# Optimization experiments

Hardware: AMD Instinct MI355X
Metric: run time of the kernel (lower is better)

Reference implementation:

```python
import jax, jax.numpy as jnp
import numpy as np

# DeltaNet single-token decode step. Hard-coded dims from the torch source:
# hidden H=2048 (chosen), qk=2048 (16h x 128 -> repeat to 32h), v=4096 (32h x 128),
# conv channels 8192, kernel 4, state [1,32,128,128].
H = 2048
EPS = 1e-6

def _l2norm(x):
    return x * jax.lax.rsqrt(jnp.sum(x * x, axis=-1, keepdims=True) + EPS)

def setup_inputs() -> dict:
    key = jax.random.key(0)
    ks = jax.random.split(key, 12)
    w = lambda k, s, sc=0.02: jax.random.normal(k, s, dtype=jnp.float32) * sc
    return {
        "x": jax.random.normal(ks[0], (1, 1, H), dtype=jnp.float32),
        "state": jax.random.normal(ks[1], (1, 32, 128, 128), dtype=jnp.float32) * 0.02,
        "conv_state": jax.random.normal(ks[2], (1, 8192, 3), dtype=jnp.float32) * 0.1,
        "W_qkv": w(ks[3], (8192, H)),
        "W_z": w(ks[4], (4096, H)),
        "W_b": w(ks[5], (32, H)),
        "W_a": w(ks[6], (32, H)),
        "conv_w": w(ks[7], (8192, 1, 4), 0.3),
        "A_log": jax.random.uniform(ks[8], (32,), minval=-2.0, maxval=0.0, dtype=jnp.float32),
        "dt_bias": w(ks[9], (32,), 0.5),
        "norm_w": jnp.ones((128,), jnp.float32),
        "W_out": w(ks[10], (H, 4096)),
    }

def reference(x, state, conv_state, W_qkv, W_z, W_b, W_a, conv_w, A_log, dt_bias, norm_w, W_out):
    # projections (bias-free Linear, torch convention y = x @ W.T)
    mixed = jnp.einsum('blh,ch->blc', x, W_qkv)           # [1,1,8192]
    z = jnp.einsum('blh,ch->blc', x, W_z).reshape(1, 1, 32, 128)
    beta = jax.nn.sigmoid(jnp.einsum('blh,ch->blc', x, W_b))  # [1,1,32]
    a = jnp.einsum('blh,ch->blc', x, W_a)                 # [1,1,32]

    # depthwise causal conv (groups=8192, kernel 4, output length 1)
    combined = jnp.concatenate([conv_state, mixed.transpose(0, 2, 1)], axis=-1)  # [1,8192,4]
    new_conv = combined[:, :, -3:]
    conv_out = jnp.sum(combined * conv_w[None, :, 0, :], axis=-1)  # [1,8192]
    mixed = jax.nn.silu(conv_out)[:, None, :]             # [1,1,8192]

    q, k, v = mixed[..., :2048], mixed[..., 2048:4096], mixed[..., 4096:]
    q = jnp.repeat(q.reshape(1, 1, 16, 128), 2, axis=2)   # [1,1,32,128]
    k = jnp.repeat(k.reshape(1, 1, 16, 128), 2, axis=2)
    v = v.reshape(1, 1, 32, 128)

    g = -jnp.exp(A_log) * jax.nn.softplus(a + dt_bias)    # [1,1,32]

    q = _l2norm(q)[:, 0] / jnp.sqrt(jnp.float32(128.0))   # [1,32,128]
    k = _l2norm(k)[:, 0]
    v = v[:, 0]
    g_t = jnp.exp(g[:, 0])[..., None, None]               # [1,32,1,1]
    beta_t = beta[:, 0][..., None]                        # [1,32,1]

    # gated delta-rule state update
    s = state * g_t                                       # [1,32,128,128]
    kv_mem = jnp.einsum('bhkv,bhk->bhv', s, k)            # [1,32,128]
    delta = (v - kv_mem) * beta_t
    new_state = s + k[..., None] * delta[..., None, :]    # [1,32,128,128]
    out = jnp.einsum('bhkv,bhk->bhv', new_state, q)       # [1,32,128]

    # gated RMSNorm (Mamba2-style: rmsnorm(x * silu(z)) * w)
    out_flat = out.reshape(-1, 128)
    z_flat = z.reshape(-1, 128)
    gated = out_flat * jax.nn.silu(z_flat)
    out_flat = gated * jax.lax.rsqrt(jnp.mean(gated * gated, axis=-1, keepdims=True) + EPS) * norm_w

    out = jnp.einsum('blc,hc->blh', out_flat.reshape(1, 1, 4096), W_out)  # [1,1,H]
    return (out, new_state, new_conv)
```

## Files before the change

kernel.cpp:

```cpp
#include <hip/hip_runtime.h>
#include <math.h>

__global__ __launch_bounds__(256) void k_gemv_in(
    const float* __restrict__ x,
    const float* __restrict__ Wqkv,
    const float* __restrict__ Wz,
    const float* __restrict__ Wb,
    const float* __restrict__ Wa,
    float* __restrict__ mixed, float* __restrict__ zb,
    float* __restrict__ b_raw, float* __restrict__ a_raw)
{
  const int tid  = threadIdx.x;
  const int lane = tid & 63;
  const int wave = tid >> 6;

  float4 xr[8];
  #pragma unroll
  for (int j = 0; j < 8; j++)
    xr[j] = *(const float4*)(x + j*256 + lane*4);

  const int row0 = blockIdx.x * 16 + wave * 4;
  for (int rr = 0; rr < 4; rr++){
    const int row = row0 + rr;
    const float* W; float* dst;
    if (row < 8192)       { W = Wqkv + (size_t)row * 2048;          dst = mixed + row; }
    else if (row < 12288) { W = Wz   + (size_t)(row-8192) * 2048;   dst = zb + (row-8192); }
    else if (row < 12320) { W = Wb   + (size_t)(row-12288) * 2048;  dst = b_raw + (row-12288); }
    else                  { W = Wa   + (size_t)(row-12320) * 2048;  dst = a_raw + (row-12320); }
    float acc = 0.f;
    #pragma unroll
    for (int j = 0; j < 8; j++){
      float4 w = *(const float4*)(W + j*256 + lane*4);
      acc += w.x*xr[j].x + w.y*xr[j].y + w.z*xr[j].z + w.w*xr[j].w;
    }
    #pragma unroll
    for (int off = 32; off >= 1; off >>= 1) acc += __shfl_xor(acc, off, 64);
    if (lane == 0) *dst = acc;
  }
}

__global__ __launch_bounds__(256) void k_conv(
    const float* __restrict__ conv_state,
    const float* __restrict__ conv_w,
    const float* __restrict__ mixed,
    float* __restrict__ act,
    float* __restrict__ new_conv)
{
  const int c = blockIdx.x * 256 + threadIdx.x;
  const float cs0 = conv_state[c*3+0];
  const float cs1 = conv_state[c*3+1];
  const float cs2 = conv_state[c*3+2];
  const float m   = mixed[c];
  const float w0 = conv_w[c*4+0];
  const float w1 = conv_w[c*4+1];
  const float w2 = conv_w[c*4+2];
  const float w3 = conv_w[c*4+3];
  const float co = cs0*w0 + cs1*w1 + cs2*w2 + m*w3;
  act[c] = co / (1.f + expf(-co));
  new_conv[c*3+0] = cs1;
  new_conv[c*3+1] = cs2;
  new_conv[c*3+2] = m;
}

__global__ __launch_bounds__(128) void k_head(
    const float* __restrict__ act,
    const float* __restrict__ zbuf,
    const float* __restrict__ b_raw,
    const float* __restrict__ a_raw,
    const float* __restrict__ A_log,
    const float* __restrict__ dt_bias,
    const float* __restrict__ norm_w,
    const float* __restrict__ state,
    float* __restrict__ new_state,
    float* __restrict__ out_flat)
{
  const int h = blockIdx.x;
  const int t = threadIdx.x;
  const int hb = h >> 1;
  const int lane = t & 63, wid = t >> 6;

  __shared__ float qn[128], kn[128];
  __shared__ float red[4];

  const float qv = act[hb*128 + t];
  const float kv = act[2048 + hb*128 + t];
  const float vv = act[4096 + h*128 + t];

  float sq = qv*qv, sk = kv*kv;
  #pragma unroll
  for (int off = 32; off >= 1; off >>= 1){
    sq += __shfl_xor(sq, off, 64);
    sk += __shfl_xor(sk, off, 64);
  }
  if (lane == 0){ red[wid] = sq; red[2+wid] = sk; }
  __syncthreads();
  const float qscale = rsqrtf(red[0]+red[1] + 1e-6f) * 0.088388347648318440550f;
  const float kscale = rsqrtf(red[2]+red[3] + 1e-6f);
  qn[t] = qv * qscale;
  kn[t] = kv * kscale;
  __syncthreads();

  float g_t, beta;
  {
    const float av = a_raw[h] + dt_bias[h];
    const float sp = (av > 20.f) ? av : log1pf(expf(av));
    g_t  = expf(-expf(A_log[h]) * sp);
    beta = 1.f / (1.f + expf(-b_raw[h]));
  }

  const float* st  = state     + (size_t)h * 16384;
  float*       nst = new_state + (size_t)h * 16384;

  float s[128];
  float kvm = 0.f;
  #pragma unroll
  for (int k = 0; k < 128; k++){
    s[k] = st[k*128 + t] * g_t;
    kvm += s[k] * kn[k];
  }
  const float delta = (vv - kvm) * beta;
  float oacc = 0.f;
  #pragma unroll
  for (int k = 0; k < 128; k++){
    const float ns = s[k] + kn[k] * delta;
    nst[k*128 + t] = ns;
    oacc += ns * qn[k];
  }

  const float zz = zbuf[h*128 + t];
  const float gated = oacc * (zz / (1.f + expf(-zz)));
  float s2 = gated * gated;
  #pragma unroll
  for (int off = 32; off >= 1; off >>= 1) s2 += __shfl_xor(s2, off, 64);
  if (lane == 0) red[wid] = s2;
  __syncthreads();
  const float mean = (red[0] + red[1]) * (1.f/128.f);
  out_flat[h*128 + t] = gated * rsqrtf(mean + 1e-6f) * norm_w[t];
}

__global__ __launch_bounds__(256) void k_gemv_out(
    const float* __restrict__ out_flat,
    const float* __restrict__ Wout,
    float* __restrict__ out)
{
  __shared__ float xs[4096];
  const int tid = threadIdx.x;
  #pragma unroll
  for (int i = 0; i < 16; i++) xs[tid + i*256] = out_flat[tid + i*256];
  __syncthreads();

  const int lane = tid & 63, wave = tid >> 6;
  const int row0 = blockIdx.x * 16 + wave * 4;
  for (int rr = 0; rr < 4; rr++){
    const int row = row0 + rr;
    const float* W = Wout + (size_t)row * 4096;
    float acc = 0.f;
    #pragma unroll
    for (int j = 0; j < 16; j++){
      float4 w = *(const float4*)(W + j*256 + lane*4);
      acc += w.x*xs[j*256+lane*4+0] + w.y*xs[j*256+lane*4+1]
           + w.z*xs[j*256+lane*4+2] + w.w*xs[j*256+lane*4+3];
    }
    #pragma unroll
    for (int off = 32; off >= 1; off >>= 1) acc += __shfl_xor(acc, off, 64);
    if (lane == 0) out[row] = acc;
  }
}

extern "C" void kernel_launch(void* const* d_in, const int* in_sizes, int n_in,
                              void* d_out, int out_size, void* d_ws, size_t ws_size,
                              hipStream_t stream) {
  const float* x          = (const float*)d_in[0];
  const float* state      = (const float*)d_in[1];
  const float* conv_state = (const float*)d_in[2];
  const float* W_qkv      = (const float*)d_in[3];
  const float* W_z        = (const float*)d_in[4];
  const float* W_b        = (const float*)d_in[5];
  const float* W_a        = (const float*)d_in[6];
  const float* conv_w     = (const float*)d_in[7];
  const float* A_log      = (const float*)d_in[8];
  const float* dt_bias    = (const float*)d_in[9];
  const float* norm_w     = (const float*)d_in[10];
  const float* W_out      = (const float*)d_in[11];

  float* out       = (float*)d_out;
  float* new_state = (float*)d_out + 2048;
  float* new_conv  = (float*)d_out + 2048 + 524288;

  float* ws     = (float*)d_ws;
  float* mixed  = ws;
  float* zb     = ws + 8192;
  float* b_raw  = ws + 12288;
  float* a_raw  = ws + 12320;
  float* act    = ws + 12352;
  float* oflat  = ws + 20544;

  hipLaunchKernelGGL(k_gemv_in, dim3(772), dim3(256), 0, stream,
                     x, W_qkv, W_z, W_b, W_a, mixed, zb, b_raw, a_raw);
  hipLaunchKernelGGL(k_conv, dim3(32), dim3(256), 0, stream,
                     conv_state, conv_w, mixed, act, new_conv);
  hipLaunchKernelGGL(k_head, dim3(32), dim3(128), 0, stream,
                     act, zb, b_raw, a_raw, A_log, dt_bias, norm_w,
                     state, new_state, oflat);
  hipLaunchKernelGGL(k_gemv_out, dim3(128), dim3(256), 0, stream,
                     oflat, W_out, out);
}
```

Baseline: 193.3 us.

## Fuse depthwise conv into head kernel and widen GEMV grids with two rows per wave

The separate conv kernel is removed. Each head block now computes the conv and SiLU for its own q, k and v channels and writes new_conv itself, which saves one launch and the round trip through the act buffer. Both GEMV kernels now have each wave handle two rows at once with both weight loads in flight, and the grids are doubled so more waves stream the weight matrices. The cost is that q/k conv channels are computed twice, once by each head that shares them, and the head kernel, which still runs only 32 blocks, gets more serial work.

```diff
diff --git a/kernel.cpp b/kernel.cpp
--- a/kernel.cpp
+++ b/kernel.cpp
@@ -19,51 +19,33 @@
   for (int j = 0; j < 8; j++)
     xr[j] = *(const float4*)(x + j*256 + lane*4);
 
-  const int row0 = blockIdx.x * 16 + wave * 4;
-  for (int rr = 0; rr < 4; rr++){
-    const int row = row0 + rr;
-    const float* W; float* dst;
-    if (row < 8192)       { W = Wqkv + (size_t)row * 2048;          dst = mixed + row; }
-    else if (row < 12288) { W = Wz   + (size_t)(row-8192) * 2048;   dst = zb + (row-8192); }
-    else if (row < 12320) { W = Wb   + (size_t)(row-12288) * 2048;  dst = b_raw + (row-12288); }
-    else                  { W = Wa   + (size_t)(row-12320) * 2048;  dst = a_raw + (row-12320); }
-    float acc = 0.f;
-    #pragma unroll
-    for (int j = 0; j < 8; j++){
-      float4 w = *(const float4*)(W + j*256 + lane*4);
-      acc += w.x*xr[j].x + w.y*xr[j].y + w.z*xr[j].z + w.w*xr[j].w;
-    }
-    #pragma unroll
-    for (int off = 32; off >= 1; off >>= 1) acc += __shfl_xor(acc, off, 64);
-    if (lane == 0) *dst = acc;
-  }
-}
-
-__global__ __launch_bounds__(256) void k_conv(
+  const int row0 = blockIdx.x * 8 + wave * 2;
+  const float* W; float* dst;
+  if (row0 < 8192)       { W = Wqkv + (size_t)row0 * 2048;          dst = mixed + row0; }
+  else if (row0 < 12288) { W = Wz   + (size_t)(row0-8192) * 2048;   dst = zb + (row0-8192); }
+  else if (row0 < 12320) { W = Wb   + (size_t)(row0-12288) * 2048;  dst = b_raw + (row0-12288); }
+  else                   { W = Wa   + (size_t)(row0-12320) * 2048;  dst = a_raw + (row0-12320); }
+
+  float acc0 = 0.f, acc1 = 0.f;
+  #pragma unroll
+  for (int j = 0; j < 8; j++){
+    float4 w0 = *(const float4*)(W + j*256 + lane*4);
+    float4 w1 = *(const float4*)(W + 2048 + j*256 + lane*4);
+    acc0 += w0.x*xr[j].x + w0.y*xr[j].y + w0.z*xr[j].z + w0.w*xr[j].w;
+    acc1 += w1.x*xr[j].x + w1.y*xr[j].y + w1.z*xr[j].z + w1.w*xr[j].w;
+  }
+  #pragma unroll
+  for (int off = 32; off >= 1; off >>= 1){
+    acc0 += __shfl_xor(acc0, off, 64);
+    acc1 += __shfl_xor(acc1, off, 64);
+  }
+  if (lane == 0){ dst[0] = acc0; dst[1] = acc1; }
+}
+
+__global__ __launch_bounds__(128) void k_head(
+    const float* __restrict__ mixed,
     const float* __restrict__ conv_state,
     const float* __restrict__ conv_w,
-    const float* __restrict__ mixed,
-    float* __restrict__ act,
-    float* __restrict__ new_conv)
-{
-  const int c = blockIdx.x * 256 + threadIdx.x;
-  const float cs0 = conv_state[c*3+0];
-  const float cs1 = conv_state[c*3+1];
-  const float cs2 = conv_state[c*3+2];
-  const float m   = mixed[c];
-  const float w0 = conv_w[c*4+0];
-  const float w1 = conv_w[c*4+1];
-  const float w2 = conv_w[c*4+2];
-  const float w3 = conv_w[c*4+3];
-  const float co = cs0*w0 + cs1*w1 + cs2*w2 + m*w3;
-  act[c] = co / (1.f + expf(-co));
-  new_conv[c*3+0] = cs1;
-  new_conv[c*3+1] = cs2;
-  new_conv[c*3+2] = m;
-}
-
-__global__ __launch_bounds__(128) void k_head(
-    const float* __restrict__ act,
     const float* __restrict__ zbuf,
     const float* __restrict__ b_raw,
     const float* __restrict__ a_raw,
@@ -72,6 +54,7 @@
     const float* __restrict__ norm_w,
     const float* __restrict__ state,
     float* __restrict__ new_state,
+    float* __restrict__ new_conv,
     float* __restrict__ out_flat)
 {
   const int h = blockIdx.x;
@@ -82,9 +65,31 @@
   __shared__ float qn[128], kn[128];
   __shared__ float red[4];
 
-  const float qv = act[hb*128 + t];
-  const float kv = act[2048 + hb*128 + t];
-  const float vv = act[4096 + h*128 + t];
+  const int cq = hb*128 + t;
+  const int ck = 2048 + hb*128 + t;
+  const int cv = 4096 + h*128 + t;
+  float qv, kv, vv;
+  {
+    float c0, c1, c2, m, w0, w1, w2, w3, co;
+    c0 = conv_state[cq*3+0]; c1 = conv_state[cq*3+1]; c2 = conv_state[cq*3+2];
+    m  = mixed[cq];
+    w0 = conv_w[cq*4+0]; w1 = conv_w[cq*4+1]; w2 = conv_w[cq*4+2]; w3 = conv_w[cq*4+3];
+    co = c0*w0 + c1*w1 + c2*w2 + m*w3;
+    qv = co / (1.f + expf(-co));
+    new_conv[cq*3+0] = c1; new_conv[cq*3+1] = c2; new_conv[cq*3+2] = m;
+    c0 = conv_state[ck*3+0]; c1 = conv_state[ck*3+1]; c2 = conv_state[ck*3+2];
+    m  = mixed[ck];
+    w0 = conv_w[ck*4+0]; w1 = conv_w[ck*4+1]; w2 = conv_w[ck*4+2]; w3 = conv_w[ck*4+3];
+    co = c0*w0 + c1*w1 + c2*w2 + m*w3;
+    kv = co / (1.f + expf(-co));
+    new_conv[ck*3+0] = c1; new_conv[ck*3+1] = c2; new_conv[ck*3+2] = m;
+    c0 = conv_state[cv*3+0]; c1 = conv_state[cv*3+1]; c2 = conv_state[cv*3+2];
+    m  = mixed[cv];
+    w0 = conv_w[cv*4+0]; w1 = conv_w[cv*4+1]; w2 = conv_w[cv*4+2]; w3 = conv_w[cv*4+3];
+    co = c0*w0 + c1*w1 + c2*w2 + m*w3;
+    vv = co / (1.f + expf(-co));
+    new_conv[cv*3+0] = c1; new_conv[cv*3+1] = c2; new_conv[cv*3+2] = m;
+  }
 
   float sq = qv*qv, sk = kv*kv;
   #pragma unroll
@@ -146,25 +151,29 @@
   __shared__ float xs[4096];
   const int tid = threadIdx.x;
   #pragma unroll
-  for (int i = 0; i < 16; i++) xs[tid + i*256] = out_flat[tid + i*256];
+  for (int i = 0; i < 4; i++)
+    *(float4*)(xs + tid*4 + i*1024) = *(const float4*)(out_flat + tid*4 + i*1024);
   __syncthreads();
 
   const int lane = tid & 63, wave = tid >> 6;
-  const int row0 = blockIdx.x * 16 + wave * 4;
-  for (int rr = 0; rr < 4; rr++){
-    const int row = row0 + rr;
-    const float* W = Wout + (size_t)row * 4096;
-    float acc = 0.f;
-    #pragma unroll
-    for (int j = 0; j < 16; j++){
-      float4 w = *(const float4*)(W + j*256 + lane*4);
-      acc += w.x*xs[j*256+lane*4+0] + w.y*xs[j*256+lane*4+1]
-           + w.z*xs[j*256+lane*4+2] + w.w*xs[j*256+lane*4+3];
-    }
-    #pragma unroll
-    for (int off = 32; off >= 1; off >>= 1) acc += __shfl_xor(acc, off, 64);
-    if (lane == 0) out[row] = acc;
-  }
+  const int row0 = blockIdx.x * 8 + wave * 2;
+  const float* W0 = Wout + (size_t)row0 * 4096;
+  float acc0 = 0.f, acc1 = 0.f;
+  #pragma unroll
+  for (int j = 0; j < 16; j++){
+    float4 w0 = *(const float4*)(W0 + j*256 + lane*4);
+    float4 w1 = *(const float4*)(W0 + 4096 + j*256 + lane*4);
+    const float x0 = xs[j*256+lane*4+0], x1 = xs[j*256+lane*4+1];
+    const float x2 = xs[j*256+lane*4+2], x3 = xs[j*256+lane*4+3];
+    acc0 += w0.x*x0 + w0.y*x1 + w0.z*x2 + w0.w*x3;
+    acc1 += w1.x*x0 + w1.y*x1 + w1.z*x2 + w1.w*x3;
+  }
+  #pragma unroll
+  for (int off = 32; off >= 1; off >>= 1){
+    acc0 += __shfl_xor(acc0, off, 64);
+    acc1 += __shfl_xor(acc1, off, 64);
+  }
+  if (lane == 0){ out[row0] = acc0; out[row0+1] = acc1; }
 }
 
 extern "C" void kernel_launch(void* const* d_in, const int* in_sizes, int n_in,
@@ -192,16 +201,13 @@
   float* zb     = ws + 8192;
   float* b_raw  = ws + 12288;
   float* a_raw  = ws + 12320;
-  float* act    = ws + 12352;
-  float* oflat  = ws + 20544;
-
-  hipLaunchKernelGGL(k_gemv_in, dim3(772), dim3(256), 0, stream,
+  float* oflat  = ws + 12352;
+
+  hipLaunchKernelGGL(k_gemv_in, dim3(1544), dim3(256), 0, stream,
                      x, W_qkv, W_z, W_b, W_a, mixed, zb, b_raw, a_raw);
-  hipLaunchKernelGGL(k_conv, dim3(32), dim3(256), 0, stream,
-                     conv_state, conv_w, mixed, act, new_conv);
   hipLaunchKernelGGL(k_head, dim3(32), dim3(128), 0, stream,
-                     act, zb, b_raw, a_raw, A_log, dt_bias, norm_w,
-                     state, new_state, oflat);
-  hipLaunchKernelGGL(k_gemv_out, dim3(128), dim3(256), 0, stream,
+                     mixed, conv_state, conv_w, zb, b_raw, a_raw, A_log, dt_bias,
+                     norm_w, state, new_state, new_conv, oflat);
+  hipLaunchKernelGGL(k_gemv_out, dim3(256), dim3(256), 0, stream,
                      oflat, W_out, out);
 }
```

Result: faster. 180.6 us (-6.6%).
